# Kernel tuning notes

Measured on AMD Instinct MI355X. Metric: run time of the kernel, lower is better.

Reference implementation:

```python
import jax, jax.numpy as jnp
import numpy as np
from itertools import permutations, combinations

BATCH = 32768
EPS = 1e-06  # positivity eps from __init__


def _levi_civita7():
    e = np.zeros((7,) * 7, dtype=np.float32)
    for p in permutations(range(7)):
        inv = sum(1 for i in range(7) for j in range(i + 1, 7) if p[i] > p[j])
        e[p] = -1.0 if inv % 2 else 1.0
    return jnp.asarray(e)

_EPS7 = _levi_civita7()  # (7,7,7,7,7,7,7) rank-7 Levi-Civita tensor
_TRIPLES = np.array(list(combinations(range(7), 3)), dtype=np.int32)  # (35,3) i<j<k index triples
_PERMS3 = [((0, 1, 2), 1.0), ((1, 2, 0), 1.0), ((2, 0, 1), 1.0),
           ((0, 2, 1), -1.0), ((2, 1, 0), -1.0), ((1, 0, 2), -1.0)]


def _phi_full(phi):
    # expand 35 independent components to fully antisymmetric (B,7,7,7)
    b = phi.shape[0]
    pf = jnp.zeros((b, 7, 7, 7), phi.dtype)
    for perm, s in _PERMS3:
        ia = _TRIPLES[:, perm[0]]
        ib = _TRIPLES[:, perm[1]]
        ic = _TRIPLES[:, perm[2]]
        pf = pf.at[:, ia, ib, ic].set(s * phi)
    return pf


def _metric_from_phi(phi):
    # Standard G2 metric: B_ij = (1/144) phi_ikl phi_jmn phi_pqr eps^{klmnpqr};
    # g = B / |det B|^{1/9}  (unit-determinant normalization)
    pf = _phi_full(phi)  # (B,7,7,7)
    C = jnp.einsum('klmnpqr,bpqr->bklmn', _EPS7, pf)  # (B,7,7,7,7)
    T = jnp.einsum('bklmn,bjmn->bklj', C, pf)          # (B,7,7,7)
    Bm = jnp.einsum('bikl,bklj->bij', pf, T) / 144.0   # (B,7,7)
    det = jnp.linalg.det(Bm)
    g = Bm / (jnp.abs(det)[:, None, None] + 1e-12) ** (1.0 / 9.0)
    return 0.5 * (g + jnp.swapaxes(g, -1, -2))  # exact symmetry for eigvalsh


def setup_inputs() -> dict:
    key = jax.random.key(0)
    phi = jax.random.normal(key, (BATCH, 35), dtype=jnp.float32)
    return {"phi": phi}


def reference(phi):
    g = _metric_from_phi(phi)              # (B,7,7)
    ev = jnp.linalg.eigvalsh(g)            # (B,7)
    return jax.nn.relu(-ev + EPS).sum(axis=-1)  # (B,) sum of negative-eigenvalue violations
```

## Files before the change

kernel.cpp:

```cpp
#include <hip/hip_runtime.h>
#include <utility>

#define BATCH 32768
#define NPHI 35

typedef float v2f __attribute__((ext_vector_type(2)));

constexpr int choose2(int n){ return (n*(n-1))/2; }

constexpr int tri_id_sorted(int a,int b,int c){
  int id=0;
  for(int x=0;x<a;++x) id += choose2(6-x);
  for(int y=a+1;y<b;++y) id += (6-y);
  id += (c-b-1);
  return id;
}

constexpr int tri_id3(int a,int b,int c){
  int x=a,y=b,z=c;
  if (x>y){int t=x;x=y;y=t;}
  if (y>z){int t=y;y=z;z=t;}
  if (x>y){int t=x;x=y;y=t;}
  return tri_id_sorted(x,y,z);
}

constexpr int sgn3(int a,int b,int c){
  int inv = (a>b)+(a>c)+(b>c);
  return (inv&1)? -1 : 1;
}

constexpr int UT(int i,int j){
  return i*7 - (i*(i-1))/2 + (j-i);
}

constexpr int PAIR(int k,int l){
  return k*7 - (k*(k+1))/2 + (l - k - 1);
}

struct Prog {
  int n;
  unsigned char kind[1472];
  unsigned char init[1472];
  short         dst [1472];
  unsigned char a   [1472];
  short         b   [1472];
  signed char   s   [1472];
  unsigned char grp [1472];
};

constexpr Prog build_prog(){
  Prog P{}; P.n=0;
  for(int k=0;k<7;++k) for(int l=k+1;l<7;++l){
    const int kl = PAIR(k,l);
    bool tinit[7]={};
    for(int m=0;m<7;++m) for(int n2=m+1;n2<7;++n2){
      if(m==k||m==l||n2==k||n2==l) continue;
      int comp[3]={0,0,0}; int cn=0;
      for(int x=0;x<7;++x) if(x!=k&&x!=l&&x!=m&&x!=n2){ comp[cn]=x; ++cn; }
      int perm[7]={k,l,m,n2,comp[0],comp[1],comp[2]};
      int invc=0;
      for(int i=0;i<7;++i) for(int j=i+1;j<7;++j) if(perm[i]>perm[j]) ++invc;
      const int es=(invc&1)? -1 : 1;
      const int tcomp=tri_id_sorted(comp[0],comp[1],comp[2]);
      for(int j=0;j<7;++j){
        if(j==m||j==n2) continue;
        P.kind[P.n]=0;
        P.init[P.n]=tinit[j]?0:1; tinit[j]=true;
        P.dst [P.n]=(short)(kl*7+j);
        P.a   [P.n]=(unsigned char)tcomp;
        P.b   [P.n]=(short)tri_id3(j,m,n2);
        P.s   [P.n]=(signed char)(es*sgn3(j,m,n2));
        P.grp [P.n]=(unsigned char)kl;
        ++P.n;
      }
    }
    for(int i=0;i<7;++i){
      if(i==k||i==l) continue;
      for(int j=i;j<7;++j){
        P.kind[P.n]=1;
        P.init[P.n]=0;
        P.dst [P.n]=(short)UT(i,j);
        P.a   [P.n]=(unsigned char)tri_id3(i,k,l);
        P.b   [P.n]=(short)(kl*7+j);
        P.s   [P.n]=(signed char)sgn3(i,k,l);
        P.grp [P.n]=(unsigned char)kl;
        ++P.n;
      }
    }
  }
  return P;
}

static constexpr Prog PROG = build_prog();
static_assert(PROG.n == 1470, "program size unexpected");

constexpr int PHASE_OF[21] = {
  3,3,3,3, 0, 1, 3,3, 0, 2, 1, 0, 0, 2, 2, 0, 2, 1, 2, 1, 1
};

template<int PH, int Q>
__device__ __forceinline__ void step_if(float (&T)[147], float (&U)[28],
                                        const float (&ph)[NPHI]){
  if constexpr (PHASE_OF[PROG.grp[Q]] == PH){
    if constexpr (Q > 0 && PROG.kind[Q] != PROG.kind[Q-1]) {
      __builtin_amdgcn_sched_barrier(0);
    }
    constexpr int  d = PROG.dst[Q];
    constexpr int  a = PROG.a[Q];
    constexpr int  b = PROG.b[Q];
    constexpr bool neg  = (PROG.s[Q] < 0);
    constexpr bool init = (PROG.init[Q] != 0);
    if constexpr (PROG.kind[Q] == 0){
      const float x = neg ? -ph[a] : ph[a];
      if constexpr (init) T[d] = x * ph[b];
      else                T[d] = fmaf(x, ph[b], T[d]);
    } else {
      const float x = neg ? -ph[a] : ph[a];
      U[d] = fmaf(x, T[b], U[d]);
    }
  }
}

template<int PH, int... Q>
__device__ __forceinline__ void run_phase(float (&T)[147], float (&U)[28],
                                          const float (&ph)[NPHI],
                                          std::integer_sequence<int, Q...>){
  (step_if<PH, Q>(T, U, ph), ...);
}

#define ROT_BODY(p1, q1, GUARD)                                               \
  {                                                                           \
    const float apq = A[UT(p1,q1)];                                           \
    const float app = A[UT(p1,p1)];                                           \
    const float aqq = A[UT(q1,q1)];                                           \
    bool doit = true;                                                         \
    if (GUARD) doit = __any(fabsf(apq) > 1e-6f*(fabsf(app)+fabsf(aqq)));      \
    if (doit) {                                                               \
      float d = 2.0f*apq;                                                     \
      d = d + ((d >= 0.0f)? 1e-30f : -1e-30f);                                \
      const float tau = (aqq - app) * __builtin_amdgcn_rcpf(d);               \
      float t = __builtin_amdgcn_rcpf(                                        \
                  fabsf(tau) + __builtin_amdgcn_sqrtf(fmaf(tau,tau,1.0f)));   \
      t = (tau >= 0.0f)? t : -t;                                              \
      const float c = __builtin_amdgcn_rsqf(fmaf(t,t,1.0f));                  \
      const float s = t*c;                                                    \
      A[UT(p1,p1)] = fmaf(-t, apq, app);                                      \
      A[UT(q1,q1)] = fmaf( t, apq, aqq);                                      \
      A[UT(p1,q1)] = 0.0f;                                                    \
      const v2f cs  = {  c, s };                                              \
      const v2f msc = { -s, c };                                              \
      _Pragma("unroll")                                                       \
      for (int r=0;r<7;++r){                                                  \
        if (r==p1 || r==q1) continue;                                         \
        const int irp = (r<p1)? UT(r,p1) : UT(p1,r);                          \
        const int irq = (r<q1)? UT(r,q1) : UT(q1,r);                          \
        const v2f arp2 = { A[irp], A[irp] };                                  \
        const v2f arq2 = { A[irq], A[irq] };                                  \
        const v2f res = __builtin_elementwise_fma(cs, arp2, msc*arq2);        \
        A[irp] = res.x;                                                       \
        A[irq] = res.y;                                                       \
      }                                                                       \
    }                                                                         \
  }

__global__ __launch_bounds__(256,2)
void PositivityConstraint_89086211654295_kernel(const float* __restrict__ phi,
                                                float* __restrict__ out){
  const int wv  = threadIdx.x >> 6;
  const int ln  = threadIdx.x & 63;
  const int gid = blockIdx.x*64 + ln;

  __shared__ float Upart[3][64][30];

  const float* __restrict__ p = phi + (size_t)gid * NPHI;
  float ph[NPHI];
  {
    const float4* __restrict__ p4 = reinterpret_cast<const float4*>(p);
    #pragma unroll
    for (int k=0;k<8;++k){
      const float4 v = p4[k];
      ph[4*k+0]=v.x; ph[4*k+1]=v.y; ph[4*k+2]=v.z; ph[4*k+3]=v.w;
    }
    ph[32]=p[32]; ph[33]=p[33]; ph[34]=p[34];
  }

  float T[147];
  float U[28];
  #pragma unroll
  for (int i=0;i<28;++i) U[i] = 0.0f;

  switch (wv){
    case 0: run_phase<0>(T,U,ph, std::make_integer_sequence<int,PROG.n>{}); break;
    case 1: run_phase<1>(T,U,ph, std::make_integer_sequence<int,PROG.n>{}); break;
    case 2: run_phase<2>(T,U,ph, std::make_integer_sequence<int,PROG.n>{}); break;
    default:run_phase<3>(T,U,ph, std::make_integer_sequence<int,PROG.n>{}); break;
  }

  if (wv){
    v2f* __restrict__ row = reinterpret_cast<v2f*>(&Upart[wv-1][ln][0]);
    #pragma unroll
    for (int k=0;k<14;++k){ v2f t = { U[2*k], U[2*k+1] }; row[k] = t; }
  }
  __syncthreads();
  if (wv) return;

  #pragma unroll
  for (int h=0;h<3;++h){
    const v2f* __restrict__ row = reinterpret_cast<const v2f*>(&Upart[h][ln][0]);
    #pragma unroll
    for (int k=0;k<14;++k){
      const v2f t = row[k];
      U[2*k]   += t.x;
      U[2*k+1] += t.y;
    }
  }

  float A[28];
  #pragma unroll
  for (int i=0;i<28;++i) A[i] = U[i]*(1.0f/6.0f);

  #pragma unroll 1
  for (int sweep=0; sweep<4; ++sweep){
    #pragma unroll
    for (int p1=0;p1<7;++p1){
      #pragma unroll
      for (int q1=p1+1;q1<7;++q1){
        ROT_BODY(p1, q1, false)
      }
    }
  }
  {
    #pragma unroll
    for (int p1=0;p1<7;++p1){
      #pragma unroll
      for (int q1=p1+1;q1<7;++q1){
        ROT_BODY(p1, q1, true)
      }
    }
  }

  float det = 1.0f;
  #pragma unroll
  for (int i=0;i<7;++i) det *= A[UT(i,i)];
  const float ad = fabsf(det) + 1e-12f;
  const float scale = __builtin_amdgcn_exp2f(__builtin_amdgcn_logf(ad) * (1.0f/9.0f));
  const float inv = __builtin_amdgcn_rcpf(scale);

  float sum = 0.0f;
  #pragma unroll
  for (int i=0;i<7;++i){
    const float ev = A[UT(i,i)]*inv;
    const float r = 1e-6f - ev;
    sum += fmaxf(r, 0.0f);
  }
  out[gid] = sum;
}

extern "C" void kernel_launch(void* const* d_in, const int* in_sizes, int n_in,
                              void* d_out, int out_size, void* d_ws, size_t ws_size,
                              hipStream_t stream) {
  const float* phi = (const float*)d_in[0];
  float* out = (float*)d_out;
  (void)in_sizes; (void)n_in; (void)out_size; (void)d_ws; (void)ws_size;
  hipLaunchKernelGGL(PositivityConstraint_89086211654295_kernel,
                     dim3(BATCH/64), dim3(256), 0, stream, phi, out);
}
```

Before: 67.26 us.

## Split metric contraction across two waves and rewrite Jacobi rotation formulas

Changes the per-sample work split from four wavefronts to two, assigning the 21 contraction groups 11/10 to the waves. Shared-memory reduction shrinks to one partial and blocks become 128 threads. The Jacobi rotation angle computation is reformulated to use rsqrt and sqrt of half-angle cosine with a sign-bit trick instead of tau-based division. This reduces cross-wave reduction and synchronisation cost, but each wave carries more serial FMA work and fewer waves are resident for latency hiding.

```diff
diff --git a/kernel.cpp b/kernel.cpp
--- a/kernel.cpp
+++ b/kernel.cpp
@@ -95,7 +95,8 @@
 static_assert(PROG.n == 1470, "program size unexpected");
 
 constexpr int PHASE_OF[21] = {
-  3,3,3,3, 0, 1, 3,3, 0, 2, 1, 0, 0, 2, 2, 0, 2, 1, 2, 1, 1
+  0,0,0,0,0,0,0,0,0,0,0,
+  1,1,1,1,1,1,1,1,1,1
 };
 
 template<int PH, int Q>
@@ -136,19 +137,24 @@
     bool doit = true;                                                         \
     if (GUARD) doit = __any(fabsf(apq) > 1e-6f*(fabsf(app)+fabsf(aqq)));      \
     if (doit) {                                                               \
-      float d = 2.0f*apq;                                                     \
-      d = d + ((d >= 0.0f)? 1e-30f : -1e-30f);                                \
-      const float tau = (aqq - app) * __builtin_amdgcn_rcpf(d);               \
-      float t = __builtin_amdgcn_rcpf(                                        \
-                  fabsf(tau) + __builtin_amdgcn_sqrtf(fmaf(tau,tau,1.0f)));   \
-      t = (tau >= 0.0f)? t : -t;                                              \
-      const float c = __builtin_amdgcn_rsqf(fmaf(t,t,1.0f));                  \
-      const float s = t*c;                                                    \
+      const float x   = aqq - app;                                            \
+      const float y   = apq + apq;                                            \
+      const float ax  = fabsf(x) + 1e-18f;                                    \
+      const float ss  = fmaf(ax, ax, y*y);                   \
+      const float w   = __builtin_amdgcn_rsqf(ss);                   \
+      const float u   = ax * w;                           \
+      const float r1  = ss * w;                             \
+      const float c   = __builtin_amdgcn_sqrtf(fmaf(0.5f, u, 0.5f));          \
+      const float tm  = fabsf(y) * __builtin_amdgcn_rcpf(ax + r1);   \
+      const unsigned sb = (__float_as_uint(x) ^ __float_as_uint(y))           \
+                          & 0x80000000u;                                      \
+      const float t   = __uint_as_float(__float_as_uint(tm) ^ sb);            \
+      const float s1  = t * c;                                                \
       A[UT(p1,p1)] = fmaf(-t, apq, app);                                      \
       A[UT(q1,q1)] = fmaf( t, apq, aqq);                                      \
       A[UT(p1,q1)] = 0.0f;                                                    \
-      const v2f cs  = {  c, s };                                              \
-      const v2f msc = { -s, c };                                              \
+      const v2f cs2 = {  c, s1 };                                             \
+      const v2f msc = { -s1, c };                                             \
       _Pragma("unroll")                                                       \
       for (int r=0;r<7;++r){                                                  \
         if (r==p1 || r==q1) continue;                                         \
@@ -156,21 +162,21 @@
         const int irq = (r<q1)? UT(r,q1) : UT(q1,r);                          \
         const v2f arp2 = { A[irp], A[irp] };                                  \
         const v2f arq2 = { A[irq], A[irq] };                                  \
-        const v2f res = __builtin_elementwise_fma(cs, arp2, msc*arq2);        \
+        const v2f res = __builtin_elementwise_fma(cs2, arp2, msc*arq2);       \
         A[irp] = res.x;                                                       \
         A[irq] = res.y;                                                       \
       }                                                                       \
     }                                                                         \
   }
 
-__global__ __launch_bounds__(256,2)
+__global__ __launch_bounds__(128,1)
 void PositivityConstraint_89086211654295_kernel(const float* __restrict__ phi,
                                                 float* __restrict__ out){
   const int wv  = threadIdx.x >> 6;
   const int ln  = threadIdx.x & 63;
   const int gid = blockIdx.x*64 + ln;
 
-  __shared__ float Upart[3][64][30];
+  __shared__ float Upart[64][30];
 
   const float* __restrict__ p = phi + (size_t)gid * NPHI;
   float ph[NPHI];
@@ -189,24 +195,19 @@
   #pragma unroll
   for (int i=0;i<28;++i) U[i] = 0.0f;
 
-  switch (wv){
-    case 0: run_phase<0>(T,U,ph, std::make_integer_sequence<int,PROG.n>{}); break;
-    case 1: run_phase<1>(T,U,ph, std::make_integer_sequence<int,PROG.n>{}); break;
-    case 2: run_phase<2>(T,U,ph, std::make_integer_sequence<int,PROG.n>{}); break;
-    default:run_phase<3>(T,U,ph, std::make_integer_sequence<int,PROG.n>{}); break;
-  }
-
-  if (wv){
-    v2f* __restrict__ row = reinterpret_cast<v2f*>(&Upart[wv-1][ln][0]);
+  if (wv == 0){
+    run_phase<0>(T,U,ph, std::make_integer_sequence<int,PROG.n>{});
+  } else {
+    run_phase<1>(T,U,ph, std::make_integer_sequence<int,PROG.n>{});
+    v2f* __restrict__ row = reinterpret_cast<v2f*>(&Upart[ln][0]);
     #pragma unroll
     for (int k=0;k<14;++k){ v2f t = { U[2*k], U[2*k+1] }; row[k] = t; }
   }
   __syncthreads();
   if (wv) return;
 
-  #pragma unroll
-  for (int h=0;h<3;++h){
-    const v2f* __restrict__ row = reinterpret_cast<const v2f*>(&Upart[h][ln][0]);
+  {
+    const v2f* __restrict__ row = reinterpret_cast<const v2f*>(&Upart[ln][0]);
     #pragma unroll
     for (int k=0;k<14;++k){
       const v2f t = row[k];
@@ -263,5 +264,5 @@
   float* out = (float*)d_out;
   (void)in_sizes; (void)n_in; (void)out_size; (void)d_ws; (void)ws_size;
   hipLaunchKernelGGL(PositivityConstraint_89086211654295_kernel,
-                     dim3(BATCH/64), dim3(256), 0, stream, phi, out);
-}
+                     dim3(BATCH/64), dim3(128), 0, stream, phi, out);
+}
```

New measurement: 62.74 us. 1.07x faster.
